# Kernel optimization log

Measured on AMD Instinct MI355X. Metric: run time of the kernel, lower is better.

Reference implementation:

```python
import jax, jax.numpy as jnp
import numpy as np

SIGMA2 = 1.9 * 1.9   # LJ sigma^2 (Angstrom^2)
EPS = 0.2            # LJ well depth
R2_SOFT = 0.25       # softening to keep energies finite for random dofs


def _local_ht(dofs):
    """dofs [..., 9] -> local homogeneous transform [..., 4, 4].
    Uses (phi, theta, d) bond-style dofs: R = Rz(phi) @ Ry(theta),
    translation d along the rotated x-axis."""
    phi, theta = dofs[..., 0], dofs[..., 1]
    d = 1.5 + 0.25 * jnp.tanh(dofs[..., 2])  # bond length ~1.25..1.75 A
    cp, sp = jnp.cos(phi), jnp.sin(phi)
    ct, st = jnp.cos(theta), jnp.sin(theta)
    r00, r01, r02 = cp * ct, -sp, cp * st
    r10, r11, r12 = sp * ct, cp, sp * st
    r20, r21, r22 = -st, jnp.zeros_like(ct), ct
    tx, ty, tz = d * r00, d * r10, d * r20
    zero, one = jnp.zeros_like(phi), jnp.ones_like(phi)
    ht = jnp.stack([
        jnp.stack([r00, r01, r02, tx], -1),
        jnp.stack([r10, r11, r12, ty], -1),
        jnp.stack([r20, r21, r22, tz], -1),
        jnp.stack([zero, zero, zero, one], -1),
    ], -2)
    return ht


def _forward_kin(full_dofs, P, A):
    # per-pose chain kinforest: cumulative left-product of local HTs
    ht = _local_ht(full_dofs.reshape(P, A, 9))  # [P, A, 4, 4]
    compose = lambda a, b: jnp.einsum('...ij,...jk->...ik', a, b)
    cum = jax.lax.associative_scan(compose, ht, axis=1)
    return cum[..., :3, 3].reshape(-1, 3)  # [P*A, 3]


def _lj_score(coords):
    # coords [P, A, 3] -> per-pose softened LJ energy [P]
    sq = jnp.sum(coords * coords, axis=-1)                 # [P, A]
    G = jnp.einsum('pad,pbd->pab', coords, coords)         # [P, A, A] GEMM
    r2 = sq[:, :, None] + sq[:, None, :] - 2.0 * G + R2_SOFT
    inv6 = (SIGMA2 / r2) ** 3
    e = 4.0 * EPS * (inv6 * inv6 - inv6)
    A = coords.shape[1]
    mask = jnp.triu(jnp.ones((A, A), dtype=coords.dtype), k=1)  # i < j
    return jnp.sum(e * mask, axis=(1, 2))


def setup_inputs() -> dict:
    key = jax.random.key(0)
    k1, k2 = jax.random.split(key)
    P, A = 4, 4096
    full_dofs = 0.5 * jax.random.normal(k1, (P * A, 9), dtype=jnp.float32)
    pose_stack_coords = 5.0 * jax.random.normal(k2, (P, A, 3), dtype=jnp.float32)
    kinforest_id = jnp.arange(P * A, dtype=jnp.int64)
    return {"full_dofs": full_dofs, "pose_stack_coords": pose_stack_coords,
            "kinforest_id": kinforest_id}


def reference(full_dofs, pose_stack_coords, kinforest_id):
    P, A, _ = pose_stack_coords.shape
    kincoords = _forward_kin(full_dofs, P, A)  # [P*A, 3]
    coords = pose_stack_coords.reshape(-1, 3).at[kinforest_id].set(kincoords)
    coords = coords.reshape(P, A, 3)
    return _lj_score(coords)  # [P]
```

## Files before the change

### kernel.cpp

```cpp
#include <hip/hip_runtime.h>
#include <math.h>

#define A_ATOMS 4096
#define P_POSES 4
#define N_TOT   (A_ATOMS * P_POSES)
#define TILE    128
#define NTILES  (A_ATOMS / TILE)
#define NPAIRT  (NTILES * (NTILES + 1) / 2)

#define SEG     64
#define NSEG    (A_ATOMS / SEG)

typedef float v2f __attribute__((ext_vector_type(2)));

__device__ __constant__ float c_SIGMA2  = 1.9f * 1.9f;
__device__ __constant__ float c_4EPS    = 0.8f;
__device__ __constant__ float c_R2SOFT  = 0.25f;

struct RT { float m[12]; };

__device__ inline RT rt_identity() {
    RT v;
    v.m[0]=1.f; v.m[1]=0.f; v.m[2]=0.f;  v.m[3]=0.f;
    v.m[4]=0.f; v.m[5]=1.f; v.m[6]=0.f;  v.m[7]=0.f;
    v.m[8]=0.f; v.m[9]=0.f; v.m[10]=1.f; v.m[11]=0.f;
    return v;
}

__device__ inline RT rt_compose(const RT& a, const RT& b) {
    RT c;
#pragma unroll
    for (int i = 0; i < 3; ++i) {
        float a0 = a.m[i*4+0], a1 = a.m[i*4+1], a2 = a.m[i*4+2];
        c.m[i*4+0] = fmaf(a0, b.m[0], fmaf(a1, b.m[4],  a2*b.m[8]));
        c.m[i*4+1] = fmaf(a0, b.m[1], fmaf(a1, b.m[5],  a2*b.m[9]));
        c.m[i*4+2] = fmaf(a0, b.m[2], fmaf(a1, b.m[6],  a2*b.m[10]));
        c.m[i*4+3] = fmaf(a0, b.m[3], fmaf(a1, b.m[7],  fmaf(a2, b.m[11], a.m[i*4+3])));
    }
    return c;
}

__device__ inline RT rt_shfl_up(const RT& a, int off) {
    RT r;
#pragma unroll
    for (int i = 0; i < 12; ++i) r.m[i] = __shfl_up(a.m[i], off, 64);
    return r;
}

__device__ inline RT local_ht(const float* __restrict__ dof) {
    float phi = dof[0], th = dof[1];
    float d = fmaf(0.25f, tanhf(dof[2]), 1.5f);
    float sp, cp, st, ct;
    sincosf(phi, &sp, &cp);
    sincosf(th,  &st, &ct);
    RT h;
    h.m[0] = cp*ct; h.m[1] = -sp; h.m[2]  = cp*st; h.m[3]  = d*cp*ct;
    h.m[4] = sp*ct; h.m[5] =  cp; h.m[6]  = sp*st; h.m[7]  = d*sp*ct;
    h.m[8] = -st;   h.m[9] = 0.f; h.m[10] = ct;    h.m[11] = -d*st;
    return h;
}

__global__ __launch_bounds__(SEG) void fk_scan(const float* __restrict__ dofs,
                                               float4* __restrict__ R0,
                                               float4* __restrict__ R1,
                                               float4* __restrict__ R2,
                                               float4* __restrict__ S0,
                                               float4* __restrict__ S1,
                                               float4* __restrict__ S2) {
    const int pose = blockIdx.x >> 6;
    const int seg  = blockIdx.x & (NSEG - 1);
    const int lane = threadIdx.x;
    const int atom = seg * SEG + lane;
    const int g    = pose * A_ATOMS + atom;

    RT v = local_ht(dofs + (size_t)g * 9);

#pragma unroll
    for (int off = 1; off < 64; off <<= 1) {
        RT l = rt_shfl_up(v, off);
        if (lane >= off) v = rt_compose(l, v);
    }

    R0[g] = make_float4(v.m[0], v.m[1], v.m[2],  v.m[3]);
    R1[g] = make_float4(v.m[4], v.m[5], v.m[6],  v.m[7]);
    R2[g] = make_float4(v.m[8], v.m[9], v.m[10], v.m[11]);

    if (lane == 63) {
        int s = pose * NSEG + seg;
        S0[s] = make_float4(v.m[0], v.m[1], v.m[2],  v.m[3]);
        S1[s] = make_float4(v.m[4], v.m[5], v.m[6],  v.m[7]);
        S2[s] = make_float4(v.m[8], v.m[9], v.m[10], v.m[11]);
    }
}

__global__ __launch_bounds__(512) void fk_apply(const int* __restrict__ kid,
                                                const float4* __restrict__ R0,
                                                const float4* __restrict__ R1,
                                                const float4* __restrict__ R2,
                                                const float4* __restrict__ S0,
                                                const float4* __restrict__ S1,
                                                const float4* __restrict__ S2,
                                                float* __restrict__ X,
                                                float* __restrict__ Y,
                                                float* __restrict__ Z,
                                                float* __restrict__ out) {
    __shared__ float4 e0[NSEG], e1[NSEG], e2[NSEG];

    const int pose = blockIdx.x;
    const int tid  = threadIdx.x;
    if (tid == 0) out[pose] = 0.f;

    if (tid < 64) {
        int s = pose * NSEG + tid;
        float4 a0 = S0[s], a1 = S1[s], a2 = S2[s];
        RT v;
        v.m[0]=a0.x; v.m[1]=a0.y; v.m[2]=a0.z;  v.m[3]=a0.w;
        v.m[4]=a1.x; v.m[5]=a1.y; v.m[6]=a1.z;  v.m[7]=a1.w;
        v.m[8]=a2.x; v.m[9]=a2.y; v.m[10]=a2.z; v.m[11]=a2.w;
#pragma unroll
        for (int off = 1; off < 64; off <<= 1) {
            RT l = rt_shfl_up(v, off);
            if (tid >= off) v = rt_compose(l, v);
        }
        RT ex = rt_shfl_up(v, 1);
        if (tid == 0) ex = rt_identity();
        e0[tid] = make_float4(ex.m[0], ex.m[1], ex.m[2],  ex.m[3]);
        e1[tid] = make_float4(ex.m[4], ex.m[5], ex.m[6],  ex.m[7]);
        e2[tid] = make_float4(ex.m[8], ex.m[9], ex.m[10], ex.m[11]);
    }
    __syncthreads();

#pragma unroll
    for (int k = 0; k < A_ATOMS / 512; ++k) {
        int a = tid + k * 512;
        int g = pose * A_ATOMS + a;
        float4 r0 = R0[g], r1 = R1[g], r2 = R2[g];
        float4 x0 = e0[a >> 6], x1 = e1[a >> 6], x2 = e2[a >> 6];
        float tx = fmaf(x0.x, r0.w, fmaf(x0.y, r1.w, fmaf(x0.z, r2.w, x0.w)));
        float ty = fmaf(x1.x, r0.w, fmaf(x1.y, r1.w, fmaf(x1.z, r2.w, x1.w)));
        float tz = fmaf(x2.x, r0.w, fmaf(x2.y, r1.w, fmaf(x2.z, r2.w, x2.w)));
        int dst = kid[g];
        X[dst] = tx; Y[dst] = ty; Z[dst] = tz;
    }
}

__global__ __launch_bounds__(256) void lj_kernel(const float* __restrict__ X,
                                                 const float* __restrict__ Y,
                                                 const float* __restrict__ Z,
                                                 float* __restrict__ out) {
    const int pose = blockIdx.y;
    int rr = blockIdx.x, bi = 0;
    while (rr >= NTILES - bi) { rr -= NTILES - bi; ++bi; }
    const int bj = bi + rr;

    __shared__ float sxi[TILE], syi[TILE], szi[TILE];
    __shared__ float sxj[TILE], syj[TILE], szj[TILE];

    const int tid = threadIdx.x;
    const float* Xp = X + pose * A_ATOMS;
    const float* Yp = Y + pose * A_ATOMS;
    const float* Zp = Z + pose * A_ATOMS;

    if (tid < TILE) {
        int gi = bi * TILE + tid;
        sxi[tid] = Xp[gi]; syi[tid] = Yp[gi]; szi[tid] = Zp[gi];
    } else {
        int t = tid - TILE;
        int gj = bj * TILE + t;
        sxj[t] = Xp[gj]; syj[t] = Yp[gj]; szj[t] = Zp[gj];
    }
    __syncthreads();

    const int i0 = (tid & 15) * 8;
    const int j0 = (tid >> 4) * 8;

    const float SIG2 = c_SIGMA2, SOFT = c_R2SOFT;
    float acc = 0.f;

    if (bi != bj) {
        float xi[8], yi[8], zi[8];
#pragma unroll
        for (int k = 0; k < 8; ++k) {
            xi[k] = sxi[i0 + k]; yi[k] = syi[i0 + k]; zi[k] = szi[i0 + k];
        }
        v2f xj2[4], yj2[4], zj2[4];
#pragma unroll
        for (int p = 0; p < 4; ++p) {
            xj2[p] = (v2f){sxj[j0 + 2*p], sxj[j0 + 2*p + 1]};
            yj2[p] = (v2f){syj[j0 + 2*p], syj[j0 + 2*p + 1]};
            zj2[p] = (v2f){szj[j0 + 2*p], szj[j0 + 2*p + 1]};
        }
        const v2f soft2 = (v2f){SOFT, SOFT};
        v2f acc2 = (v2f){0.f, 0.f};
#pragma unroll
        for (int p = 0; p < 4; ++p) {
#pragma unroll
            for (int k = 0; k < 8; ++k) {
                v2f dx = xi[k] - xj2[p];
                v2f dy = yi[k] - yj2[p];
                v2f dz = zi[k] - zj2[p];
                v2f r2 = __builtin_elementwise_fma(dx, dx,
                         __builtin_elementwise_fma(dy, dy,
                         __builtin_elementwise_fma(dz, dz, soft2)));
                v2f rc = (v2f){__builtin_amdgcn_rcpf(r2.x), __builtin_amdgcn_rcpf(r2.y)};
                v2f t  = SIG2 * rc;
                v2f i6 = t * t * t;
                acc2 += __builtin_elementwise_fma(i6, i6, -i6);
            }
        }
        acc = acc2.x + acc2.y;
    } else {
        float xi[8], yi[8], zi[8], xj[8], yj[8], zj[8];
#pragma unroll
        for (int k = 0; k < 8; ++k) {
            xi[k] = sxi[i0 + k]; yi[k] = syi[i0 + k]; zi[k] = szi[i0 + k];
            xj[k] = sxj[j0 + k]; yj[k] = syj[j0 + k]; zj[k] = szj[j0 + k];
        }
#pragma unroll
        for (int jj = 0; jj < 8; ++jj) {
            int j = j0 + jj;
#pragma unroll
            for (int k = 0; k < 8; ++k) {
                float dx = xi[k] - xj[jj], dy = yi[k] - yj[jj], dz = zi[k] - zj[jj];
                float r2 = fmaf(dx, dx, fmaf(dy, dy, fmaf(dz, dz, SOFT)));
                float t  = SIG2 * __builtin_amdgcn_rcpf(r2);
                float i6 = t * t * t;
                float hh = fmaf(i6, i6, -i6);
                acc += ((i0 + k) < j) ? hh : 0.f;
            }
        }
    }
    acc *= c_4EPS;

#pragma unroll
    for (int off = 32; off > 0; off >>= 1) acc += __shfl_down(acc, off, 64);

    __shared__ float wsum[4];
    int lane = tid & 63, wid = tid >> 6;
    if (lane == 0) wsum[wid] = acc;
    __syncthreads();
    if (tid == 0) {
        float s = wsum[0] + wsum[1] + wsum[2] + wsum[3];
        atomicAdd(out + pose, s);
    }
}

extern "C" void kernel_launch(void* const* d_in, const int* in_sizes, int n_in,
                              void* d_out, int out_size, void* d_ws, size_t ws_size,
                              hipStream_t stream) {
    (void)in_sizes; (void)n_in; (void)out_size; (void)ws_size;
    const float* dofs = (const float*)d_in[0];
    const int*   kid  = (const int*)d_in[2];
    float*       out  = (float*)d_out;

    float* X = (float*)d_ws;
    float* Y = X + N_TOT;
    float* Z = Y + N_TOT;
    float4* R0 = (float4*)(Z + N_TOT);
    float4* R1 = R0 + N_TOT;
    float4* R2 = R1 + N_TOT;
    float4* S0 = R2 + N_TOT;
    float4* S1 = S0 + P_POSES * NSEG;
    float4* S2 = S1 + P_POSES * NSEG;

    fk_scan<<<P_POSES * NSEG, SEG, 0, stream>>>(dofs, R0, R1, R2, S0, S1, S2);
    fk_apply<<<P_POSES, 512, 0, stream>>>(kid, R0, R1, R2, S0, S1, S2, X, Y, Z, out);
    dim3 grid(NPAIRT, P_POSES);
    lj_kernel<<<grid, 256, 0, stream>>>(X, Y, Z, out);
}
```

Before: 94.82 us.

## Fuse forward-kinematics segment scan and apply into one per-pose kernel

```diff
diff --git a/kernel.cpp b/kernel.cpp
--- a/kernel.cpp
+++ b/kernel.cpp
@@ -10,6 +10,8 @@
 
 #define SEG     64
 #define NSEG    (A_ATOMS / SEG)
+#define FKF_T   1024
+#define SPW     (NSEG / (FKF_T / 64))
 
 typedef float v2f __attribute__((ext_vector_type(2)));
 
@@ -60,59 +62,44 @@
     return h;
 }
 
-__global__ __launch_bounds__(SEG) void fk_scan(const float* __restrict__ dofs,
-                                               float4* __restrict__ R0,
-                                               float4* __restrict__ R1,
-                                               float4* __restrict__ R2,
-                                               float4* __restrict__ S0,
-                                               float4* __restrict__ S1,
-                                               float4* __restrict__ S2) {
-    const int pose = blockIdx.x >> 6;
-    const int seg  = blockIdx.x & (NSEG - 1);
-    const int lane = threadIdx.x;
-    const int atom = seg * SEG + lane;
-    const int g    = pose * A_ATOMS + atom;
-
-    RT v = local_ht(dofs + (size_t)g * 9);
-
-#pragma unroll
-    for (int off = 1; off < 64; off <<= 1) {
-        RT l = rt_shfl_up(v, off);
-        if (lane >= off) v = rt_compose(l, v);
-    }
-
-    R0[g] = make_float4(v.m[0], v.m[1], v.m[2],  v.m[3]);
-    R1[g] = make_float4(v.m[4], v.m[5], v.m[6],  v.m[7]);
-    R2[g] = make_float4(v.m[8], v.m[9], v.m[10], v.m[11]);
-
-    if (lane == 63) {
-        int s = pose * NSEG + seg;
-        S0[s] = make_float4(v.m[0], v.m[1], v.m[2],  v.m[3]);
-        S1[s] = make_float4(v.m[4], v.m[5], v.m[6],  v.m[7]);
-        S2[s] = make_float4(v.m[8], v.m[9], v.m[10], v.m[11]);
-    }
-}
-
-__global__ __launch_bounds__(512) void fk_apply(const int* __restrict__ kid,
-                                                const float4* __restrict__ R0,
-                                                const float4* __restrict__ R1,
-                                                const float4* __restrict__ R2,
-                                                const float4* __restrict__ S0,
-                                                const float4* __restrict__ S1,
-                                                const float4* __restrict__ S2,
-                                                float* __restrict__ X,
-                                                float* __restrict__ Y,
-                                                float* __restrict__ Z,
-                                                float* __restrict__ out) {
-    __shared__ float4 e0[NSEG], e1[NSEG], e2[NSEG];
+__global__ __launch_bounds__(FKF_T) void fk_fused(const float* __restrict__ dofs,
+                                                  const int* __restrict__ kid,
+                                                  float* __restrict__ X,
+                                                  float* __restrict__ Y,
+                                                  float* __restrict__ Z,
+                                                  float* __restrict__ out) {
+    __shared__ float4 st0[NSEG], st1[NSEG], st2[NSEG];
+    __shared__ float4 e0[NSEG],  e1[NSEG],  e2[NSEG];
 
     const int pose = blockIdx.x;
     const int tid  = threadIdx.x;
+    const int lane = tid & 63;
+    const int w    = tid >> 6;
     if (tid == 0) out[pose] = 0.f;
 
+    float tx_r[SPW], ty_r[SPW], tz_r[SPW];
+
+#pragma unroll
+    for (int i = 0; i < SPW; ++i) {
+        const int seg = w * SPW + i;
+        const int g   = pose * A_ATOMS + seg * SEG + lane;
+        RT v = local_ht(dofs + (size_t)g * 9);
+#pragma unroll
+        for (int off = 1; off < 64; off <<= 1) {
+            RT l = rt_shfl_up(v, off);
+            if (lane >= off) v = rt_compose(l, v);
+        }
+        tx_r[i] = v.m[3]; ty_r[i] = v.m[7]; tz_r[i] = v.m[11];
+        if (lane == 63) {
+            st0[seg] = make_float4(v.m[0], v.m[1], v.m[2],  v.m[3]);
+            st1[seg] = make_float4(v.m[4], v.m[5], v.m[6],  v.m[7]);
+            st2[seg] = make_float4(v.m[8], v.m[9], v.m[10], v.m[11]);
+        }
+    }
+    __syncthreads();
+
     if (tid < 64) {
-        int s = pose * NSEG + tid;
-        float4 a0 = S0[s], a1 = S1[s], a2 = S2[s];
+        float4 a0 = st0[tid], a1 = st1[tid], a2 = st2[tid];
         RT v;
         v.m[0]=a0.x; v.m[1]=a0.y; v.m[2]=a0.z;  v.m[3]=a0.w;
         v.m[4]=a1.x; v.m[5]=a1.y; v.m[6]=a1.z;  v.m[7]=a1.w;
@@ -131,14 +118,13 @@
     __syncthreads();
 
 #pragma unroll
-    for (int k = 0; k < A_ATOMS / 512; ++k) {
-        int a = tid + k * 512;
-        int g = pose * A_ATOMS + a;
-        float4 r0 = R0[g], r1 = R1[g], r2 = R2[g];
-        float4 x0 = e0[a >> 6], x1 = e1[a >> 6], x2 = e2[a >> 6];
-        float tx = fmaf(x0.x, r0.w, fmaf(x0.y, r1.w, fmaf(x0.z, r2.w, x0.w)));
-        float ty = fmaf(x1.x, r0.w, fmaf(x1.y, r1.w, fmaf(x1.z, r2.w, x1.w)));
-        float tz = fmaf(x2.x, r0.w, fmaf(x2.y, r1.w, fmaf(x2.z, r2.w, x2.w)));
+    for (int i = 0; i < SPW; ++i) {
+        const int seg = w * SPW + i;
+        const int g   = pose * A_ATOMS + seg * SEG + lane;
+        float4 x0 = e0[seg], x1 = e1[seg], x2 = e2[seg];
+        float tx = fmaf(x0.x, tx_r[i], fmaf(x0.y, ty_r[i], fmaf(x0.z, tz_r[i], x0.w)));
+        float ty = fmaf(x1.x, tx_r[i], fmaf(x1.y, ty_r[i], fmaf(x1.z, tz_r[i], x1.w)));
+        float tz = fmaf(x2.x, tx_r[i], fmaf(x2.y, ty_r[i], fmaf(x2.z, tz_r[i], x2.w)));
         int dst = kid[g];
         X[dst] = tx; Y[dst] = ty; Z[dst] = tz;
     }
@@ -256,15 +242,8 @@
     float* X = (float*)d_ws;
     float* Y = X + N_TOT;
     float* Z = Y + N_TOT;
-    float4* R0 = (float4*)(Z + N_TOT);
-    float4* R1 = R0 + N_TOT;
-    float4* R2 = R1 + N_TOT;
-    float4* S0 = R2 + N_TOT;
-    float4* S1 = S0 + P_POSES * NSEG;
-    float4* S2 = S1 + P_POSES * NSEG;
-
-    fk_scan<<<P_POSES * NSEG, SEG, 0, stream>>>(dofs, R0, R1, R2, S0, S1, S2);
-    fk_apply<<<P_POSES, 512, 0, stream>>>(kid, R0, R1, R2, S0, S1, S2, X, Y, Z, out);
+
+    fk_fused<<<P_POSES, FKF_T, 0, stream>>>(dofs, kid, X, Y, Z, out);
     dim3 grid(NPAIRT, P_POSES);
     lj_kernel<<<grid, 256, 0, stream>>>(X, Y, Z, out);
 }
```

Measured after the change: 103.7 us. 1.09x slower.

## Store only translations from FK scan and spread apply kernel across more blocks

Applied to the files above, without the earlier changes.

```diff
diff --git a/kernel.cpp b/kernel.cpp
--- a/kernel.cpp
+++ b/kernel.cpp
@@ -10,6 +10,8 @@
 
 #define SEG     64
 #define NSEG    (A_ATOMS / SEG)
+#define APPLY_T 256
+#define APPLY_B (A_ATOMS / APPLY_T)
 
 typedef float v2f __attribute__((ext_vector_type(2)));
 
@@ -61,17 +63,16 @@
 }
 
 __global__ __launch_bounds__(SEG) void fk_scan(const float* __restrict__ dofs,
-                                               float4* __restrict__ R0,
-                                               float4* __restrict__ R1,
-                                               float4* __restrict__ R2,
+                                               float* __restrict__ Tx,
+                                               float* __restrict__ Ty,
+                                               float* __restrict__ Tz,
                                                float4* __restrict__ S0,
                                                float4* __restrict__ S1,
                                                float4* __restrict__ S2) {
     const int pose = blockIdx.x >> 6;
     const int seg  = blockIdx.x & (NSEG - 1);
     const int lane = threadIdx.x;
-    const int atom = seg * SEG + lane;
-    const int g    = pose * A_ATOMS + atom;
+    const int g    = pose * A_ATOMS + seg * SEG + lane;
 
     RT v = local_ht(dofs + (size_t)g * 9);
 
@@ -81,9 +82,7 @@
         if (lane >= off) v = rt_compose(l, v);
     }
 
-    R0[g] = make_float4(v.m[0], v.m[1], v.m[2],  v.m[3]);
-    R1[g] = make_float4(v.m[4], v.m[5], v.m[6],  v.m[7]);
-    R2[g] = make_float4(v.m[8], v.m[9], v.m[10], v.m[11]);
+    Tx[g] = v.m[3]; Ty[g] = v.m[7]; Tz[g] = v.m[11];
 
     if (lane == 63) {
         int s = pose * NSEG + seg;
@@ -93,22 +92,23 @@
     }
 }
 
-__global__ __launch_bounds__(512) void fk_apply(const int* __restrict__ kid,
-                                                const float4* __restrict__ R0,
-                                                const float4* __restrict__ R1,
-                                                const float4* __restrict__ R2,
-                                                const float4* __restrict__ S0,
-                                                const float4* __restrict__ S1,
-                                                const float4* __restrict__ S2,
-                                                float* __restrict__ X,
-                                                float* __restrict__ Y,
-                                                float* __restrict__ Z,
-                                                float* __restrict__ out) {
+__global__ __launch_bounds__(APPLY_T) void fk_apply(const int* __restrict__ kid,
+                                                    const float* __restrict__ Tx,
+                                                    const float* __restrict__ Ty,
+                                                    const float* __restrict__ Tz,
+                                                    const float4* __restrict__ S0,
+                                                    const float4* __restrict__ S1,
+                                                    const float4* __restrict__ S2,
+                                                    float* __restrict__ X,
+                                                    float* __restrict__ Y,
+                                                    float* __restrict__ Z,
+                                                    float* __restrict__ out) {
     __shared__ float4 e0[NSEG], e1[NSEG], e2[NSEG];
 
-    const int pose = blockIdx.x;
+    const int pose = blockIdx.y;
+    const int blk  = blockIdx.x;
     const int tid  = threadIdx.x;
-    if (tid == 0) out[pose] = 0.f;
+    if (blk == 0 && tid == 0) out[pose] = 0.f;
 
     if (tid < 64) {
         int s = pose * NSEG + tid;
@@ -130,18 +130,15 @@
     }
     __syncthreads();
 
-#pragma unroll
-    for (int k = 0; k < A_ATOMS / 512; ++k) {
-        int a = tid + k * 512;
-        int g = pose * A_ATOMS + a;
-        float4 r0 = R0[g], r1 = R1[g], r2 = R2[g];
-        float4 x0 = e0[a >> 6], x1 = e1[a >> 6], x2 = e2[a >> 6];
-        float tx = fmaf(x0.x, r0.w, fmaf(x0.y, r1.w, fmaf(x0.z, r2.w, x0.w)));
-        float ty = fmaf(x1.x, r0.w, fmaf(x1.y, r1.w, fmaf(x1.z, r2.w, x1.w)));
-        float tz = fmaf(x2.x, r0.w, fmaf(x2.y, r1.w, fmaf(x2.z, r2.w, x2.w)));
-        int dst = kid[g];
-        X[dst] = tx; Y[dst] = ty; Z[dst] = tz;
-    }
+    const int a = blk * APPLY_T + tid;
+    const int g = pose * A_ATOMS + a;
+    float rx = Tx[g], ry = Ty[g], rz = Tz[g];
+    float4 x0 = e0[a >> 6], x1 = e1[a >> 6], x2 = e2[a >> 6];
+    float tx = fmaf(x0.x, rx, fmaf(x0.y, ry, fmaf(x0.z, rz, x0.w)));
+    float ty = fmaf(x1.x, rx, fmaf(x1.y, ry, fmaf(x1.z, rz, x1.w)));
+    float tz = fmaf(x2.x, rx, fmaf(x2.y, ry, fmaf(x2.z, rz, x2.w)));
+    int dst = kid[g];
+    X[dst] = tx; Y[dst] = ty; Z[dst] = tz;
 }
 
 __global__ __launch_bounds__(256) void lj_kernel(const float* __restrict__ X,
@@ -253,18 +250,19 @@
     const int*   kid  = (const int*)d_in[2];
     float*       out  = (float*)d_out;
 
-    float* X = (float*)d_ws;
-    float* Y = X + N_TOT;
-    float* Z = Y + N_TOT;
-    float4* R0 = (float4*)(Z + N_TOT);
-    float4* R1 = R0 + N_TOT;
-    float4* R2 = R1 + N_TOT;
-    float4* S0 = R2 + N_TOT;
+    float* X  = (float*)d_ws;
+    float* Y  = X + N_TOT;
+    float* Z  = Y + N_TOT;
+    float* Tx = Z + N_TOT;
+    float* Ty = Tx + N_TOT;
+    float* Tz = Ty + N_TOT;
+    float4* S0 = (float4*)(Tz + N_TOT);
     float4* S1 = S0 + P_POSES * NSEG;
     float4* S2 = S1 + P_POSES * NSEG;
 
-    fk_scan<<<P_POSES * NSEG, SEG, 0, stream>>>(dofs, R0, R1, R2, S0, S1, S2);
-    fk_apply<<<P_POSES, 512, 0, stream>>>(kid, R0, R1, R2, S0, S1, S2, X, Y, Z, out);
+    fk_scan<<<P_POSES * NSEG, SEG, 0, stream>>>(dofs, Tx, Ty, Tz, S0, S1, S2);
+    dim3 agrid(APPLY_B, P_POSES);
+    fk_apply<<<agrid, APPLY_T, 0, stream>>>(kid, Tx, Ty, Tz, S0, S1, S2, X, Y, Z, out);
     dim3 grid(NPAIRT, P_POSES);
     lj_kernel<<<grid, 256, 0, stream>>>(X, Y, Z, out);
 }
```

Result: faster. 90.91 us (-4.1%).
